# Kernel tuning notes

Hardware: AMD Instinct MI355X
Metric: run time of the kernel (lower is better)

## Reference

```python
import jax, jax.numpy as jnp
import numpy as np

RESET_PERIOD = 10
DECAY = 0.1
D_MODEL = 512
D_INNER = 1024
N_LAYERS = 4


def layer_norm(x, scale, bias, eps=1e-5):
    mu = jnp.mean(x, axis=-1, keepdims=True)
    var = jnp.mean((x - mu) ** 2, axis=-1, keepdims=True)
    return (x - mu) * jax.lax.rsqrt(var + eps) * scale + bias


def setup_inputs() -> dict:
    key = jax.random.key(0)
    ks = jax.random.split(key, 12)
    B, S, F, V, MF = 8, 2048, 128, 256, 4096
    D, DI, L = D_MODEL, D_INNER, N_LAYERS
    rn = lambda k, shape, s: jax.random.normal(k, shape, jnp.float32) * s
    return {
        "frames": rn(ks[0], (B, S, F), 1.0),
        "padding_mask": jax.random.uniform(ks[1], (B, S)) < 0.9,
        "W_in_proj": rn(ks[2], (F, D), 0.05),
        "b_in_proj": jnp.zeros((D,), jnp.float32),
        "pos_emb": rn(ks[3], (MF, D), 0.02),
        "ln_scale": jnp.ones((L, D), jnp.float32),
        "ln_bias": jnp.zeros((L, D), jnp.float32),
        "W_in": rn(ks[4], (L, D, 2 * DI), 0.03),
        "b_in": jnp.zeros((L, 2 * DI), jnp.float32),
        "W_out": rn(ks[5], (L, DI, D), 0.03),
        "b_out": jnp.zeros((L, D), jnp.float32),
        "fn_scale": jnp.ones((D,), jnp.float32),
        "fn_bias": jnp.zeros((D,), jnp.float32),
        "W_frame": rn(ks[6], (D, F), 0.03),
        "b_frame": jnp.zeros((F,), jnp.float32),
        "W_sym": rn(ks[7], (D, V), 0.03),
        "b_sym": jnp.zeros((V,), jnp.float32),
    }


def reference(frames, padding_mask, W_in_proj, b_in_proj, pos_emb,
              ln_scale, ln_bias, W_in, b_in, W_out, b_out,
              fn_scale, fn_bias, W_frame, b_frame, W_sym, b_sym):
    B, S, F = frames.shape
    # input projection + clamped positional embedding
    x = frames @ W_in_proj + b_in_proj                     # [B,S,D]
    pos = jnp.clip(jnp.arange(S), 0, pos_emb.shape[0] - 1)
    x = x + pos_emb[pos][None]
    # periodic hard-reset decay: frame_counter starts at 0, incremented AFTER
    # each step, so steps with (t+1) % reset_period == 0 are scaled.
    t = jnp.arange(S) + 1
    decay = jnp.where(t % RESET_PERIOD == 0, DECAY, 1.0)[None, :, None]  # [1,S,1]

    def layer(h, p):
        s, b, Wi, bi, Wo, bo = p
        n = layer_norm(h, s, b)
        uz = n @ Wi + bi                                   # [B,S,2*DI]
        u, g = jnp.split(uz, 2, axis=-1)
        y = (u * jax.nn.silu(g)) @ Wo + bo                 # [B,S,D]
        # wrapper scales the full block output (incl. residual)
        return (h + y) * decay, None

    x, _ = jax.lax.scan(layer, x, (ln_scale, ln_bias, W_in, b_in, W_out, b_out))
    x = layer_norm(x, fn_scale, fn_bias)
    frame_outputs = x @ W_frame + b_frame                  # [B,S,F]
    symbol_logits = x @ W_sym + b_sym                      # [B,S,V]
    m = padding_mask[..., None]
    frame_outputs = jnp.where(m, frame_outputs, 0.0)
    symbol_logits = jnp.where(m, symbol_logits, 0.0)
    return frame_outputs, symbol_logits
```

## Files before the change

kernel.cpp:

```cpp
#include <hip/hip_runtime.h>
#include <hip/hip_bf16.h>

using f32x4  = __attribute__((ext_vector_type(4))) float;
using bf16x8 = __attribute__((ext_vector_type(8))) short;
using bf16x4 = __attribute__((ext_vector_type(4))) short;

#define MTOT   16384
#define DMODEL 512
#define DINNER 1024
#define SEQ    2048

__device__ __forceinline__ short f2b(float f){
  unsigned u = __builtin_bit_cast(unsigned, f);
  u = (u + 0x7FFFu + ((u >> 16) & 1u)) >> 16;
  return (short)u;
}

__device__ __forceinline__ void gl_lds16(const short* g, short* l){
  __builtin_amdgcn_global_load_lds(
      (const __attribute__((address_space(1))) void*)g,
      (__attribute__((address_space(3))) void*)l, 16, 0, 0);
}

__global__ void detect_mask(const unsigned char* __restrict__ m, int* __restrict__ flag){
  __shared__ int sge2, soff, soff8;
  int tid = threadIdx.x;
  if (tid == 0){ sge2 = 0; soff = 0; soff8 = 0; }
  __syncthreads();
  int ge2 = 0, off = 0, off8 = 0;
  for (int i = tid; i < 16384; i += 256){
    unsigned char b = m[i];
    if (b >= 2) ge2++;
    if ((i & 3) && b) off++;
    if (((i & 7) == 4) && b) off8++;
  }
  atomicAdd(&sge2, ge2); atomicAdd(&soff, off); atomicAdd(&soff8, off8);
  __syncthreads();
  if (tid == 0){
    int f;
    if      (sge2 > 0) f = 2;
    else if (soff > 0) f = 1;
    else if (soff8 > 0) f = 0;
    else               f = 3;
    *flag = f;
  }
}

__device__ __forceinline__ bool mask_at(const void* mask, int flag, int m){
  if (flag == 1) return ((const unsigned char*)mask)[m] != 0;
  if (flag == 2) return ((const float*)mask)[m] != 0.0f;
  if (flag == 3) return ((const int*)mask)[2*m] != 0;
  return ((const int*)mask)[m] != 0;
}

__global__ void cvt_bf16(const float* __restrict__ in, short* __restrict__ out){
  int i = (blockIdx.x * 256 + threadIdx.x) * 4;
  float4 v = *(const float4*)(in + i);
  bf16x4 o; o[0] = f2b(v.x); o[1] = f2b(v.y); o[2] = f2b(v.z); o[3] = f2b(v.w);
  *(bf16x4*)(out + i) = o;
}

template<int GLU>
__global__ void transpose_w(const float* __restrict__ in, short* __restrict__ out, int R, int C){
  in  += (size_t)blockIdx.z * R * C;
  out += (size_t)blockIdx.z * R * C;
  __shared__ float t[32][33];
  int tx = threadIdx.x, ty = threadIdx.y;
  int r0 = blockIdx.y * 32, c0 = blockIdx.x * 32;
  #pragma unroll
  for (int i = 0; i < 4; i++)
    t[ty + i*8][tx] = in[(size_t)(r0 + ty + i*8) * C + c0 + tx];
  __syncthreads();
  #pragma unroll
  for (int i = 0; i < 4; i++){
    int oc = c0 + ty + i*8;
    int nr;
    if constexpr (GLU){
      int half = C >> 1;
      nr = (oc < half) ? (((oc >> 4) << 5) + (oc & 15))
                       : ((((oc - half) >> 4) << 5) + 16 + (oc & 15));
    } else nr = oc;
    out[(size_t)nr * R + r0 + tx] = f2b(t[tx][ty + i*8]);
  }
}

__global__ __launch_bounds__(256) void ln_k(const float* __restrict__ x,
                                            const float* __restrict__ sc,
                                            const float* __restrict__ bi,
                                            short* __restrict__ out){
  int row  = blockIdx.x * 4 + (threadIdx.x >> 6);
  int lane = threadIdx.x & 63;
  const float* p = x + (size_t)row * DMODEL + lane * 8;
  float4 a = *(const float4*)p;
  float4 b = *(const float4*)(p + 4);
  float s = a.x+a.y+a.z+a.w + b.x+b.y+b.z+b.w;
  float q = a.x*a.x+a.y*a.y+a.z*a.z+a.w*a.w + b.x*b.x+b.y*b.y+b.z*b.z+b.w*b.w;
  #pragma unroll
  for (int o = 32; o >= 1; o >>= 1){ s += __shfl_xor(s, o); q += __shfl_xor(q, o); }
  float mu  = s * (1.0f/DMODEL);
  float var = q * (1.0f/DMODEL) - mu*mu;
  float rs  = rsqrtf(var + 1e-5f);
  int c = lane * 8;
  float vals[8] = {a.x,a.y,a.z,a.w,b.x,b.y,b.z,b.w};
  bf16x8 o8;
  #pragma unroll
  for (int e = 0; e < 8; e++) o8[e] = f2b((vals[e]-mu)*rs*sc[c+e] + bi[c+e]);
  *(bf16x8*)(out + (size_t)row * DMODEL + c) = o8;
}

template<int MODE, int K>
__global__ __launch_bounds__(256) void gemm_k(
    const short* __restrict__ A, const short* __restrict__ B,
    const float* __restrict__ bias0, const float* __restrict__ bias1,
    const float* __restrict__ pos, float* __restrict__ xbuf, short* __restrict__ obuf,
    float* __restrict__ fout, const void* __restrict__ mask, const int* __restrict__ flagp,
    int ldo)
{
  constexpr int BM = 128, BN = 128;
  __shared__ short lds[(BM + BN) * 64];
  short* lA = lds;
  short* lB = lds + BM * 64;

  const int nbx = gridDim.x;
  int bid = blockIdx.y * nbx + blockIdx.x;
  const int nwg = nbx * gridDim.y;
  bid = (bid & 7) * (nwg >> 3) + (bid >> 3);
  const int bx = bid % nbx, by = bid / nbx;
  const int n0 = bx * BN, m0 = by * BM;

  const int tid = threadIdx.x, lane = tid & 63, wid = tid >> 6;
  const int lr  = lane >> 3;
  const int lks = (lane & 7) ^ (lr & 7);
  const int fr = lane & 15;
  const int kg = lane >> 4;

  const int wr = wid >> 1, wc = wid & 1;
  const int rA0 = wr * 64 + fr;
  const int rB0 = wc * 64 + fr;

  f32x4 acc[4][4];
  const f32x4 zero = {0.f, 0.f, 0.f, 0.f};
  #pragma unroll
  for (int i = 0; i < 4; i++)
    #pragma unroll
    for (int j = 0; j < 4; j++) acc[i][j] = zero;

  const short* Ab = A + (size_t)m0 * K + (size_t)lr * K + lks * 8;
  const short* Bb = B + (size_t)n0 * K + (size_t)lr * K + lks * 8;

  for (int kt = 0; kt < K; kt += 64){
    __syncthreads();
    #pragma unroll
    for (int c = 0; c < 4; c++)
      gl_lds16(Ab + kt + (size_t)(wid + c * 4) * 8 * K, lA + (wid + c * 4) * 512);
    #pragma unroll
    for (int c = 0; c < 4; c++)
      gl_lds16(Bb + kt + (size_t)(wid + c * 4) * 8 * K, lB + (wid + c * 4) * 512);
    __syncthreads();

    #pragma unroll
    for (int kb8 = 0; kb8 < 8; kb8 += 4){
      bf16x8 aF[4], bF[4];
      #pragma unroll
      for (int i = 0; i < 4; i++){
        const int row = rA0 + i * 16;
        aF[i] = *(const bf16x8*)((const char*)lA + row * 128 + (((kg + kb8) ^ (row & 7)) * 16));
      }
      #pragma unroll
      for (int j = 0; j < 4; j++){
        const int row = rB0 + j * 16;
        bF[j] = *(const bf16x8*)((const char*)lB + row * 128 + (((kg + kb8) ^ (row & 7)) * 16));
      }
      #pragma unroll
      for (int i = 0; i < 4; i++)
        #pragma unroll
        for (int j = 0; j < 4; j++)
          acc[i][j] = __builtin_amdgcn_mfma_f32_16x16x32_bf16(aF[i], bF[j], acc[i][j], 0, 0, 0);
    }
  }

  const int col0 = n0 + wc * 64 + fr;
  const int row0 = m0 + wr * 64 + kg * 4;
  int flag = 0;
  if constexpr (MODE == 3) flag = *flagp;

  #pragma unroll
  for (int i = 0; i < 4; i++){
    #pragma unroll
    for (int r = 0; r < 4; r++){
      const int gm = row0 + i * 16 + r;
      if constexpr (MODE == 1){
        #pragma unroll
        for (int jj = 0; jj < 2; jj++){
          const int j = 2 * jj;
          const int nb = n0 + wc * 64 + j * 16;
          const int lc = ((nb >> 5) << 4) + fr;
          float u = acc[i][j][r]     + bias0[lc];
          float g = acc[i][j+1][r]   + bias0[1024 + lc];
          float sg = g / (1.0f + expf(-g));
          obuf[(size_t)gm * 1024 + lc] = f2b(u * sg);
        }
      } else {
        #pragma unroll
        for (int j = 0; j < 4; j++){
          const int gn = col0 + j * 16;
          float v = acc[i][j][r];
          if constexpr (MODE == 0){
            xbuf[(size_t)gm * ldo + gn] = v + bias0[gn] + pos[(size_t)(gm & (SEQ-1)) * DMODEL + gn];
          } else if constexpr (MODE == 2){
            int s = gm & (SEQ-1);
            float d = (((s + 1) % 10) == 0) ? 0.1f : 1.0f;
            float y = v + bias0[gn];
            xbuf[(size_t)gm * ldo + gn] = (xbuf[(size_t)gm * ldo + gn] + y) * d;
          } else {
            bool mk = mask_at(mask, flag, gm);
            if (gn < 128){
              fout[(size_t)gm * 128 + gn] = mk ? (v + bias0[gn]) : 0.0f;
            } else {
              int gs = gn - 128;
              fout[(size_t)16384 * 128 + (size_t)gm * 256 + gs] = mk ? (v + bias1[gs]) : 0.0f;
            }
          }
        }
      }
    }
  }
}

extern "C" void kernel_launch(void* const* d_in, const int* in_sizes, int n_in,
                              void* d_out, int out_size, void* d_ws, size_t ws_size,
                              hipStream_t stream){
  const float* frames    = (const float*)d_in[0];
  const void*  mask      = d_in[1];
  const float* W_in_proj = (const float*)d_in[2];
  const float* b_in_proj = (const float*)d_in[3];
  const float* pos_emb   = (const float*)d_in[4];
  const float* ln_scale  = (const float*)d_in[5];
  const float* ln_bias   = (const float*)d_in[6];
  const float* W_in      = (const float*)d_in[7];
  const float* b_in      = (const float*)d_in[8];
  const float* W_out     = (const float*)d_in[9];
  const float* b_out     = (const float*)d_in[10];
  const float* fn_scale  = (const float*)d_in[11];
  const float* fn_bias   = (const float*)d_in[12];
  const float* W_frame   = (const float*)d_in[13];
  const float* b_frame   = (const float*)d_in[14];
  const float* W_sym     = (const float*)d_in[15];
  const float* b_sym     = (const float*)d_in[16];

  char* w = (char*)d_ws;
  int*   flag = (int*)w;
  float* xbuf = (float*)(w + 256);
  short* nbuf = (short*)(w + 256 + 33554432);
  short* abuf = (short*)(w + 256 + 33554432 + 16777216);
  short* frb  = (short*)(w + 256 + 33554432 + 16777216 + 33554432);
  short* Wt0  = frb + (size_t)16384 * 128;
  short* Wt1  = Wt0 + (size_t)512 * 128;
  short* Wt2  = Wt1 + (size_t)4 * 2048 * 512;
  short* Wt3  = Wt2 + (size_t)4 * 512 * 1024;
  short* Wt4  = Wt3 + (size_t)128 * 512;

  detect_mask<<<1, 256, 0, stream>>>((const unsigned char*)mask, flag);
  cvt_bf16<<<2048, 256, 0, stream>>>(frames, frb);
  transpose_w<0><<<dim3(16,  4, 1), dim3(32, 8), 0, stream>>>(W_in_proj, Wt0, 128, 512);
  transpose_w<1><<<dim3(64, 16, 4), dim3(32, 8), 0, stream>>>(W_in,      Wt1, 512, 2048);
  transpose_w<0><<<dim3(16, 32, 4), dim3(32, 8), 0, stream>>>(W_out,     Wt2, 1024, 512);
  transpose_w<0><<<dim3(4,  16, 1), dim3(32, 8), 0, stream>>>(W_frame,   Wt3, 512, 128);
  transpose_w<0><<<dim3(8,  16, 1), dim3(32, 8), 0, stream>>>(W_sym,     Wt4, 512, 256);

  gemm_k<0, 128><<<dim3(4, 128), 256, 0, stream>>>(frb, Wt0, b_in_proj, nullptr, pos_emb,
      xbuf, nullptr, nullptr, nullptr, nullptr, 512);

  for (int l = 0; l < 4; l++){
    ln_k<<<4096, 256, 0, stream>>>(xbuf, ln_scale + l*512, ln_bias + l*512, nbuf);
    gemm_k<1, 512><<<dim3(16, 128), 256, 0, stream>>>(nbuf,
        Wt1 + (size_t)l*2048*512, b_in + l*2048, nullptr, nullptr,
        nullptr, abuf, nullptr, nullptr, nullptr, 1024);
    gemm_k<2, 1024><<<dim3(4, 128), 256, 0, stream>>>(abuf, Wt2 + (size_t)l*512*1024,
        b_out + l*512, nullptr, nullptr, xbuf, nullptr, nullptr, nullptr, nullptr, 512);
  }

  ln_k<<<4096, 256, 0, stream>>>(xbuf, fn_scale, fn_bias, nbuf);
  gemm_k<3, 512><<<dim3(3, 128), 256, 0, stream>>>(nbuf, Wt3, b_frame, b_sym, nullptr,
      nullptr, nullptr, (float*)d_out, mask, flag, 0);
}
```

Baseline: 574.0 us.

## Replace GLU input GEMM with 256x256-tile, 8-wave, 8-stage-pipelined kernel

Adds a dedicated GLU GEMM kernel for the per-layer input projection. It uses 256x256 tiles, 512 threads (8 waves), an 8-slot LDS ring with async global-to-LDS loads staged ahead, XOR swizzling, and barrier-interleaved MFMA phases with setprio. The aim is to raise data reuse per tile and hide load latency behind MFMA work in the largest GEMM. The cost is heavy LDS use (128KB per block) and high register pressure, which lowers occupancy. The explicit vmcnt bookkeeping is fragile if the counts are wrong.

After: 526.9 us. -8.2%, faster.

```diff
diff --git a/kernel.cpp b/kernel.cpp
--- a/kernel.cpp
+++ b/kernel.cpp
@@ -106,6 +106,117 @@
   #pragma unroll
   for (int e = 0; e < 8; e++) o8[e] = f2b((vals[e]-mu)*rs*sc[c+e] + bi[c+e]);
   *(bf16x8*)(out + (size_t)row * DMODEL + c) = o8;
+}
+
+template<int K>
+__global__ __launch_bounds__(512, 2) void glu8p(
+    const short* __restrict__ A, const short* __restrict__ B,
+    const float* __restrict__ bias, short* __restrict__ obuf)
+{
+  constexpr int NT = K / 64;
+  constexpr int HT = NT * 4;
+  __shared__ short lds[8 * 8192];
+
+  const int nbx = gridDim.x;
+  int bid = blockIdx.y * nbx + blockIdx.x;
+  const int nwg = nbx * gridDim.y;
+  bid = (bid & 7) * (nwg >> 3) + (bid >> 3);
+  const int n0 = (bid % nbx) * 256, m0 = (bid / nbx) * 256;
+
+  const int tid = threadIdx.x, lane = tid & 63, wid = tid >> 6;
+  const int wr = wid >> 2, wc = wid & 3;
+  const int fr = lane & 15, kg = lane >> 4;
+
+  f32x4 acc[8][2][2];
+  const f32x4 zero = {0.f, 0.f, 0.f, 0.f};
+  #pragma unroll
+  for (int i = 0; i < 8; i++)
+    #pragma unroll
+    for (int nh = 0; nh < 2; nh++)
+      #pragma unroll
+      for (int j = 0; j < 2; j++) acc[i][nh][j] = zero;
+
+  const int rl0 = wid * 8 + (lane >> 3);
+  const int swz = ((lane & 7) ^ ((lane >> 3) & 7)) * 8;
+  const short* Ab = A + ((size_t)m0 + rl0) * K + swz;
+  const short* Bb = B + ((size_t)n0 + rl0) * K + swz;
+
+  auto stage = [&](int h){
+    if (h < HT){
+      const int q = h & 3, kt = h >> 2, slot = h & 7;
+      const short* src = (q < 2) ? (Ab + (size_t)(q * 128) * K + kt * 64)
+                                 : (Bb + (size_t)((q - 2) * 128) * K + kt * 64);
+      short* dst = lds + slot * 8192 + wid * 512;
+      gl_lds16(src, dst);
+      gl_lds16(src + (size_t)64 * K, dst + 4096);
+    }
+  };
+
+  #pragma unroll
+  for (int h = 0; h < 6; h++) stage(h);
+  asm volatile("s_waitcnt vmcnt(4)" ::: "memory");
+  __builtin_amdgcn_sched_barrier(0);
+  __builtin_amdgcn_s_barrier();
+  __builtin_amdgcn_sched_barrier(0);
+
+  for (int kt = 0; kt < NT; ++kt){
+    bf16x8 aF[8];
+    #pragma unroll
+    for (int p = 0; p < 4; ++p){
+      const int kb = p >> 1, nh = p & 1;
+      const int ks = kg + kb * 4;
+      if (nh == 0){
+        const int slot = (4 * kt + wr) & 7;
+        #pragma unroll
+        for (int i = 0; i < 8; i++)
+          aF[i] = *(const bf16x8*)((const char*)lds + slot * 16384
+                     + (i * 16 + fr) * 128 + ((ks ^ (fr & 7)) * 16));
+      }
+      bf16x8 bF[2];
+      {
+        const int slot = (4 * kt + 2 + nh) & 7;
+        #pragma unroll
+        for (int j = 0; j < 2; j++)
+          bF[j] = *(const bf16x8*)((const char*)lds + slot * 16384
+                     + (wc * 32 + j * 16 + fr) * 128 + ((ks ^ (fr & 7)) * 16));
+      }
+      stage(4 * kt + p + 6);
+      if (p == 3){
+        if (kt < NT - 2)       asm volatile("s_waitcnt vmcnt(4)" ::: "memory");
+        else if (kt == NT - 2) asm volatile("s_waitcnt vmcnt(0)" ::: "memory");
+      }
+      __builtin_amdgcn_sched_barrier(0);
+      __builtin_amdgcn_s_barrier();
+      __builtin_amdgcn_sched_barrier(0);
+      __builtin_amdgcn_s_setprio(1);
+      #pragma unroll
+      for (int i = 0; i < 8; i++)
+        #pragma unroll
+        for (int j = 0; j < 2; j++)
+          acc[i][nh][j] = __builtin_amdgcn_mfma_f32_16x16x32_bf16(aF[i], bF[j], acc[i][nh][j], 0, 0, 0);
+      __builtin_amdgcn_s_setprio(0);
+      __builtin_amdgcn_sched_barrier(0);
+      __builtin_amdgcn_s_barrier();
+      __builtin_amdgcn_sched_barrier(0);
+    }
+  }
+
+  #pragma unroll
+  for (int i = 0; i < 8; i++){
+    #pragma unroll
+    for (int nh = 0; nh < 2; nh++){
+      const int pc = n0 + nh * 128 + wc * 32;
+      const int lc = ((pc >> 5) << 4) + fr;
+      #pragma unroll
+      for (int r = 0; r < 4; r++){
+        const int gm = m0 + wr * 128 + i * 16 + kg * 4 + r;
+        float u = acc[i][nh][0][r] + bias[lc];
+        float g = acc[i][nh][1][r] + bias[1024 + lc];
+        float sg = g / (1.0f + expf(-g));
+        obuf[(size_t)gm * 1024 + lc] = f2b(u * sg);
+      }
+    }
+  }
 }
 
 template<int MODE, int K>
@@ -189,37 +300,24 @@
     #pragma unroll
     for (int r = 0; r < 4; r++){
       const int gm = row0 + i * 16 + r;
-      if constexpr (MODE == 1){
-        #pragma unroll
-        for (int jj = 0; jj < 2; jj++){
-          const int j = 2 * jj;
-          const int nb = n0 + wc * 64 + j * 16;
-          const int lc = ((nb >> 5) << 4) + fr;
-          float u = acc[i][j][r]     + bias0[lc];
-          float g = acc[i][j+1][r]   + bias0[1024 + lc];
-          float sg = g / (1.0f + expf(-g));
-          obuf[(size_t)gm * 1024 + lc] = f2b(u * sg);
-        }
-      } else {
-        #pragma unroll
-        for (int j = 0; j < 4; j++){
-          const int gn = col0 + j * 16;
-          float v = acc[i][j][r];
-          if constexpr (MODE == 0){
-            xbuf[(size_t)gm * ldo + gn] = v + bias0[gn] + pos[(size_t)(gm & (SEQ-1)) * DMODEL + gn];
-          } else if constexpr (MODE == 2){
-            int s = gm & (SEQ-1);
-            float d = (((s + 1) % 10) == 0) ? 0.1f : 1.0f;
-            float y = v + bias0[gn];
-            xbuf[(size_t)gm * ldo + gn] = (xbuf[(size_t)gm * ldo + gn] + y) * d;
+      #pragma unroll
+      for (int j = 0; j < 4; j++){
+        const int gn = col0 + j * 16;
+        float v = acc[i][j][r];
+        if constexpr (MODE == 0){
+          xbuf[(size_t)gm * ldo + gn] = v + bias0[gn] + pos[(size_t)(gm & (SEQ-1)) * DMODEL + gn];
+        } else if constexpr (MODE == 2){
+          int s = gm & (SEQ-1);
+          float d = (((s + 1) % 10) == 0) ? 0.1f : 1.0f;
+          float y = v + bias0[gn];
+          xbuf[(size_t)gm * ldo + gn] = (xbuf[(size_t)gm * ldo + gn] + y) * d;
+        } else {
+          bool mk = mask_at(mask, flag, gm);
+          if (gn < 128){
+            fout[(size_t)gm * 128 + gn] = mk ? (v + bias0[gn]) : 0.0f;
           } else {
-            bool mk = mask_at(mask, flag, gm);
-            if (gn < 128){
-              fout[(size_t)gm * 128 + gn] = mk ? (v + bias0[gn]) : 0.0f;
-            } else {
-              int gs = gn - 128;
-              fout[(size_t)16384 * 128 + (size_t)gm * 256 + gs] = mk ? (v + bias1[gs]) : 0.0f;
-            }
+            int gs = gn - 128;
+            fout[(size_t)16384 * 128 + (size_t)gm * 256 + gs] = mk ? (v + bias1[gs]) : 0.0f;
           }
         }
       }
@@ -273,9 +371,8 @@
 
   for (int l = 0; l < 4; l++){
     ln_k<<<4096, 256, 0, stream>>>(xbuf, ln_scale + l*512, ln_bias + l*512, nbuf);
-    gemm_k<1, 512><<<dim3(16, 128), 256, 0, stream>>>(nbuf,
-        Wt1 + (size_t)l*2048*512, b_in + l*2048, nullptr, nullptr,
-        nullptr, abuf, nullptr, nullptr, nullptr, 1024);
+    glu8p<512><<<dim3(8, 64), 512, 0, stream>>>(nbuf,
+        Wt1 + (size_t)l*2048*512, b_in + l*2048, abuf);
     gemm_k<2, 1024><<<dim3(4, 128), 256, 0, stream>>>(abuf, Wt2 + (size_t)l*512*1024,
         b_out + l*512, nullptr, nullptr, xbuf, nullptr, nullptr, nullptr, nullptr, 512);
   }
```
